# Kernel optimization log

Hardware: AMD Instinct MI355X
Metric: run time of the kernel (lower is better)

The kernel has to match this reference:

```python
import jax, jax.numpy as jnp
import numpy as np

EPS = 1e-5  # torch GroupNorm default eps


def gn(x, g, b):
    # GroupNorm with 1 group on [N, C]: normalize over channel dim per row
    mu = jnp.mean(x, axis=-1, keepdims=True)
    var = jnp.var(x, axis=-1, keepdims=True)
    return (x - mu) * jax.lax.rsqrt(var + EPS) * g + b


def setup_inputs() -> dict:
    N, A, E, D = 500000, 20000, 500000, 128
    key = jax.random.key(0)
    ks = jax.random.split(key, 12)
    s = 0.05
    return {
        "map_x": jax.random.normal(ks[0], (N, 8), jnp.float32),
        "agt_x": jax.random.normal(ks[1], (A, 80), jnp.float32),
        "u": jax.random.randint(ks[2], (E,), 0, A),
        "v": jax.random.randint(ks[3], (E,), 0, N),
        # map_fc: Linear(8,D) with bias, then custom Linear(D,D,bias=False)+GN+ReLU
        "W0": jax.random.normal(ks[4], (D, 8), jnp.float32) * s,
        "b0": jnp.zeros((D,), jnp.float32),
        "W1": jax.random.normal(ks[5], (D, D), jnp.float32) * s,
        "g1": jnp.ones((D,), jnp.float32),
        "b1": jnp.zeros((D,), jnp.float32),
        # agt_fc: Linear(80, D, bias=False)
        "Wa": jax.random.normal(ks[6], (D, 80), jnp.float32) * s,
        # self.bn GroupNorm params
        "g_bn": jnp.ones((D,), jnp.float32),
        "b_bn": jnp.zeros((D,), jnp.float32),
        # self.fc: Linear(2D, D, bias=False)+GN+ReLU
        "Wf": jax.random.normal(ks[7], (D, 2 * D), jnp.float32) * s,
        "g_fc": jnp.ones((D,), jnp.float32),
        "b_fc": jnp.zeros((D,), jnp.float32),
    }


def reference(map_x, agt_x, u, v, W0, b0, W1, g1, b1, Wa, g_bn, b_bn, Wf, g_fc, b_fc):
    # map_fc: Linear+ReLU, then Linear(no bias)+GN+ReLU
    h = jax.nn.relu(map_x @ W0.T + b0)                      # [N, D]
    h = jax.nn.relu(gn(h @ W1.T, g1, b1))                   # [N, D]
    # agent messages: project agents once (A < E), then gather per edge
    msg = (agt_x @ Wa.T)[u]                                 # [E, D]
    tmp = jnp.zeros_like(h).at[v].add(msg)                  # scatter-add into map nodes
    tmp = jax.nn.relu(gn(tmp, g_bn, b_bn))                  # [N, D]
    cat = jnp.concatenate([h, tmp], axis=-1)                # [N, 2D]
    out = jax.nn.relu(gn(cat @ Wf.T, g_fc, b_fc))           # [N, D]
    return out
```

## Files before the change

kernel.cpp:

```cpp
#include <hip/hip_runtime.h>
#include <stdint.h>

#define EPS 1e-5f

typedef short bh8 __attribute__((ext_vector_type(8)));
typedef float f4v __attribute__((ext_vector_type(4)));
typedef unsigned short ushort_t;

static __device__ __forceinline__ unsigned short f2bf(float f) {
    unsigned u = __builtin_bit_cast(unsigned, f);
    u += 0x7fffu + ((u >> 16) & 1u);
    return (unsigned short)(u >> 16);
}

static __device__ __forceinline__ float bfbits(unsigned x) {
    return __builtin_bit_cast(float, x);
}

static __device__ __forceinline__ void acc16(float* tv, uint4 qa, uint4 qb) {
    unsigned wd[8] = {qa.x, qa.y, qa.z, qa.w, qb.x, qb.y, qb.z, qb.w};
#pragma unroll
    for (int p = 0; p < 8; ++p) {
        tv[2 * p + 0] += bfbits(wd[p] << 16);
        tv[2 * p + 1] += bfbits(wd[p] & 0xffff0000u);
    }
}


__global__ void prep(const float* __restrict__ W1, const float* __restrict__ Wf,
                     const float* __restrict__ Wa, ushort_t* __restrict__ W1b,
                     ushort_t* __restrict__ Wfb, float* __restrict__ WaT) {
    int i = blockIdx.x * 256 + threadIdx.x;
    if (i < 16384) W1b[i] = f2bf(W1[i]);
    else if (i < 49152) { int j = i - 16384; Wfb[j] = f2bf(Wf[j]); }
    else if (i < 59392) { int l2 = i - 49152; int k = l2 >> 7, c = l2 & 127; WaT[l2] = Wa[c * 80 + k]; }
}

__global__ __launch_bounds__(256) void proj_agents(const float* __restrict__ agt,
                                                   const float* __restrict__ WaT,
                                                   unsigned short* __restrict__ Pb) {
    __shared__ float WT[80 * 128];
    __shared__ float xT[80][32];
    int t = threadIdx.x;
    int row0 = blockIdx.x * 32;
#pragma unroll
    for (int m = 0; m < 40; ++m) WT[t + 256 * m] = WaT[t + 256 * m];
#pragma unroll
    for (int m = 0; m < 10; ++m) {
        int f = t + 256 * m;
        int r = f / 80, k = f - r * 80;
        xT[k][r] = agt[(size_t)(row0 + r) * 80 + k];
    }
    __syncthreads();
    int tx = t & 31, ty = t >> 5;
    float acc[4][4] = {};
    for (int k = 0; k < 80; ++k) {
        float4 xv = *(const float4*)&xT[k][ty * 4];
        float4 wv = *(const float4*)&WT[k * 128 + tx * 4];
        float xa[4] = {xv.x, xv.y, xv.z, xv.w};
        float wa[4] = {wv.x, wv.y, wv.z, wv.w};
#pragma unroll
        for (int i = 0; i < 4; ++i)
#pragma unroll
            for (int j = 0; j < 4; ++j) acc[i][j] = fmaf(xa[i], wa[j], acc[i][j]);
    }
#pragma unroll
    for (int i = 0; i < 4; ++i) {
        int r = row0 + ty * 4 + i;
        union { unsigned short s[4]; uint2 q; } o;
#pragma unroll
        for (int j = 0; j < 4; ++j) o.s[j] = f2bf(acc[i][j]);
        *(uint2*)&Pb[(size_t)r * 128 + tx * 4] = o.q;
    }
}

__global__ void hist_v(const int* __restrict__ v, int* __restrict__ cnt, int E) {
    int e = blockIdx.x * 256 + threadIdx.x;
    if (e < E) atomicAdd(&cnt[v[e]], 1);
}

__global__ __launch_bounds__(256) void scan1(const int* __restrict__ cnt,
                                             int* __restrict__ rp,
                                             int* __restrict__ partials, int n) {
    __shared__ int lds[256];
    int b = blockIdx.x, t = threadIdx.x;
    int base = b * 4096 + t * 16;
    int vv[16];
    int run = 0;
#pragma unroll
    for (int i = 0; i < 16; ++i) {
        int c = (base + i < n) ? cnt[base + i] : 0;
        vv[i] = run;
        run += c;
    }
    lds[t] = run;
    __syncthreads();
#pragma unroll
    for (int off = 1; off < 256; off <<= 1) {
        int x = (t >= off) ? lds[t - off] : 0;
        __syncthreads();
        lds[t] += x;
        __syncthreads();
    }
    int excl = lds[t] - run;
    if (t == 255) partials[b] = lds[255];
#pragma unroll
    for (int i = 0; i < 16; ++i)
        if (base + i < n) rp[base + i] = excl + vv[i];
}

__global__ __launch_bounds__(256) void scan2(int* __restrict__ partials, int nb) {
    __shared__ int lds[256];
    int t = threadIdx.x;
    int vv = (t < nb) ? partials[t] : 0;
    lds[t] = vv;
    __syncthreads();
#pragma unroll
    for (int off = 1; off < 256; off <<= 1) {
        int x = (t >= off) ? lds[t - off] : 0;
        __syncthreads();
        lds[t] += x;
        __syncthreads();
    }
    if (t < nb) partials[t] = lds[t] - vv;
}

__global__ void scan3(int* __restrict__ rp, const int* __restrict__ partials,
                      int n, int E) {
    int i = blockIdx.x * 256 + threadIdx.x;
    if (i < n) rp[i] += partials[i >> 12];
    if (i == 0) rp[n] = E;
}

__global__ void fill_csr(const int* __restrict__ u, const int* __restrict__ v,
                         const int* __restrict__ rp, int* __restrict__ cursor,
                         int* __restrict__ col, int E) {
    int e = blockIdx.x * 256 + threadIdx.x;
    if (e < E) {
        int vv = v[e];
        int pos = rp[vv] + atomicAdd(&cursor[vv], 1);
        col[pos] = u[e];
    }
}

__global__ __launch_bounds__(256) void gather_gn(
    const unsigned short* __restrict__ Pb, const int* __restrict__ rp,
    const int* __restrict__ col, const float* __restrict__ g_bn,
    const float* __restrict__ b_bn, ushort_t* __restrict__ catB) {
    const int t = threadIdx.x;
    const int node = blockIdx.x * 32 + (t >> 3);
    const int c0 = (t & 7) * 16;
    const int beg = rp[node];
    const int deg = rp[node + 1] - beg;
    const int ca = col[(deg > 0) ? beg : 0];
    const int cb = col[(deg > 1) ? beg + 1 : 0];
    const int cc = col[(deg > 2) ? beg + 2 : 0];
    const int cd = col[(deg > 3) ? beg + 3 : 0];
    const unsigned short* pB = Pb + c0;
    float tv[16] = {};
    if (deg > 0) { const uint4* p = (const uint4*)(pB + (size_t)ca * 128); acc16(tv, p[0], p[1]); }
    if (deg > 1) { const uint4* p = (const uint4*)(pB + (size_t)cb * 128); acc16(tv, p[0], p[1]); }
    if (deg > 2) { const uint4* p = (const uint4*)(pB + (size_t)cc * 128); acc16(tv, p[0], p[1]); }
    if (deg > 3) { const uint4* p = (const uint4*)(pB + (size_t)cd * 128); acc16(tv, p[0], p[1]); }
    for (int k = 4; k < deg; ++k) {
        const uint4* p = (const uint4*)(pB + (size_t)col[beg + k] * 128);
        acc16(tv, p[0], p[1]);
    }
    float a = 0.f, q = 0.f;
#pragma unroll
    for (int i = 0; i < 16; ++i) { a += tv[i]; q += tv[i] * tv[i]; }
#pragma unroll
    for (int msk = 1; msk < 8; msk <<= 1) {
        a += __shfl_xor(a, msk, 64);
        q += __shfl_xor(q, msk, 64);
    }
    const float mean = a * (1.f / 128.f);
    const float var = q * (1.f / 128.f) - mean * mean;
    const float inv = rsqrtf(var + EPS);
    union { unsigned short s[16]; uint4 q4[2]; } o;
#pragma unroll
    for (int i = 0; i < 16; ++i) {
        const int cch = c0 + i;
        o.s[i] = f2bf(fmaxf((tv[i] - mean) * inv * g_bn[cch] + b_bn[cch], 0.f));
    }
    uint4* dst = (uint4*)(catB + (size_t)node * 128 + c0);
    dst[0] = o.q4[0];
    dst[1] = o.q4[1];
}

__global__ __launch_bounds__(512, 4) void fused(
    const float* __restrict__ mapx, const float* __restrict__ W0,
    const float* __restrict__ b0, const ushort_t* __restrict__ W1b,
    const float* __restrict__ g1, const float* __restrict__ b1,
    const ushort_t* __restrict__ catB, const ushort_t* __restrict__ Wfb,
    const float* __restrict__ g_fc, const float* __restrict__ b_fc,
    float* __restrict__ out, int ntiles)
{
    __shared__ __align__(16) short h0sA[32 * 128], h0sB[32 * 128];
    __shared__ __align__(16) short catsA[32 * 256], catsB[32 * 256];
    __shared__ float W0s[128 * 8];
    __shared__ float b0s[128];
    __shared__ float2 partA[8][32], partB[8][32];
    __shared__ float gA[128], bA[128], gC[128], bC[128];

    const int t = threadIdx.x;
    const int w = t >> 6;
    const int l = t & 63;
    const int l15 = l & 15, lg = l >> 4;

    if (t < 128) {
        gA[t] = g1[t];   bA[t] = b1[t];
        gC[t] = g_fc[t]; bC[t] = b_fc[t];
        b0s[t] = b0[t];
    }
    for (int i = t; i < 1024; i += 512) W0s[i] = W0[i];

    bh8 w1b[4], wfb[8];
    {
        const int wr = 16 * w + l15;
#pragma unroll
        for (int s = 0; s < 4; ++s)
            w1b[s] = *(const bh8*)(W1b + (size_t)wr * 128 + s * 32 + lg * 8);
#pragma unroll
        for (int s = 0; s < 8; ++s)
            wfb[s] = *(const bh8*)(Wfb + (size_t)wr * 256 + s * 32 + lg * 8);
    }
    __syncthreads();

    const f4v fzero = {0.f, 0.f, 0.f, 0.f};
    const int stride = (int)gridDim.x;
    const int npairs = (ntiles + 1) >> 1;

    for (int j = blockIdx.x; j < npairs; j += stride) {
        const int tileA = 2 * j, tileB = 2 * j + 1;
        const bool hasB = (tileB < ntiles);
        const int rowA0 = tileA * 32, rowB0 = tileB * 32;

        {
            const int r = t & 31, cg = t >> 5;
            const int ad = (r * 256 + cg * 16) ^ ((r & 7) << 4);
            {
                float mx[8];
                const float* p = mapx + (size_t)(rowA0 + r) * 8;
                *(float4*)&mx[0] = *(const float4*)p;
                *(float4*)&mx[4] = *(const float4*)(p + 4);
                __align__(16) unsigned short hb[8];
#pragma unroll
                for (int c = 0; c < 8; ++c) {
                    const int cc = 8 * cg + c;
                    float a = b0s[cc];
#pragma unroll
                    for (int jj = 0; jj < 8; ++jj) a = fmaf(mx[jj], W0s[cc * 8 + jj], a);
                    hb[c] = f2bf(fmaxf(a, 0.f));
                }
                *(uint4*)((char*)h0sA + ad) = *(const uint4*)&hb[0];
            }
            if (hasB) {
                float mx[8];
                const float* p = mapx + (size_t)(rowB0 + r) * 8;
                *(float4*)&mx[0] = *(const float4*)p;
                *(float4*)&mx[4] = *(const float4*)(p + 4);
                __align__(16) unsigned short hb[8];
#pragma unroll
                for (int c = 0; c < 8; ++c) {
                    const int cc = 8 * cg + c;
                    float a = b0s[cc];
#pragma unroll
                    for (int jj = 0; jj < 8; ++jj) a = fmaf(mx[jj], W0s[cc * 8 + jj], a);
                    hb[c] = f2bf(fmaxf(a, 0.f));
                }
                *(uint4*)((char*)h0sB + ad) = *(const uint4*)&hb[0];
            }
        }
        {
            const int r2 = t >> 4, cb = (t & 15) * 8;
            const int ad = (r2 * 512 + 256 + cb * 2) ^ ((r2 & 7) << 4);
            uint4 qa = *(const uint4*)(catB + (size_t)(rowA0 + r2) * 128 + cb);
            *(uint4*)((char*)catsA + ad) = qa;
            if (hasB) {
                uint4 qb = *(const uint4*)(catB + (size_t)(rowB0 + r2) * 128 + cb);
                *(uint4*)((char*)catsB + ad) = qb;
            }
        }
        __syncthreads();

        f4v a2A[2], a2B[2];
        a2A[0] = fzero; a2A[1] = fzero; a2B[0] = fzero; a2B[1] = fzero;
#pragma unroll
        for (int s = 0; s < 4; ++s) {
            bh8 afA[2], afB[2];
#pragma unroll
            for (int m = 0; m < 2; ++m) {
                const int row = 16 * m + l15;
                const int a = (row * 256 + s * 64 + lg * 16) ^ ((row & 7) << 4);
                afA[m] = *(const bh8*)((const char*)h0sA + a);
                afB[m] = *(const bh8*)((const char*)h0sB + a);
            }
#pragma unroll
            for (int m = 0; m < 2; ++m) {
                a2A[m] = __builtin_amdgcn_mfma_f32_16x16x32_bf16(w1b[s], afA[m], a2A[m], 0, 0, 0);
                a2B[m] = __builtin_amdgcn_mfma_f32_16x16x32_bf16(w1b[s], afB[m], a2B[m], 0, 0, 0);
            }
        }

#pragma unroll
        for (int m = 0; m < 2; ++m) {
            float aA = a2A[m][0] + a2A[m][1] + a2A[m][2] + a2A[m][3];
            float qA = a2A[m][0] * a2A[m][0] + a2A[m][1] * a2A[m][1] +
                       a2A[m][2] * a2A[m][2] + a2A[m][3] * a2A[m][3];
            float aB = a2B[m][0] + a2B[m][1] + a2B[m][2] + a2B[m][3];
            float qB = a2B[m][0] * a2B[m][0] + a2B[m][1] * a2B[m][1] +
                       a2B[m][2] * a2B[m][2] + a2B[m][3] * a2B[m][3];
            aA += __shfl_xor(aA, 16, 64); qA += __shfl_xor(qA, 16, 64);
            aA += __shfl_xor(aA, 32, 64); qA += __shfl_xor(qA, 32, 64);
            aB += __shfl_xor(aB, 16, 64); qB += __shfl_xor(qB, 16, 64);
            aB += __shfl_xor(aB, 32, 64); qB += __shfl_xor(qB, 32, 64);
            if (lg == 0) {
                partA[w][16 * m + l15] = make_float2(aA, qA);
                partB[w][16 * m + l15] = make_float2(aB, qB);
            }
        }
        __syncthreads();

#pragma unroll
        for (int m = 0; m < 2; ++m) {
            const int row = 16 * m + l15;
            const int c00 = 16 * w + 4 * lg;
            const int ad = (row * 512 + c00 * 2) ^ ((row & 7) << 4);
            {
                float a = 0.f, q = 0.f;
#pragma unroll
                for (int pw = 0; pw < 8; ++pw) {
                    float2 pq = partA[pw][row];
                    a += pq.x; q += pq.y;
                }
                const float mean = a * (1.f / 128.f);
                const float var = q * (1.f / 128.f) - mean * mean;
                const float inv = rsqrtf(var + EPS);
                union { unsigned short s[4]; uint2 q2; } o;
#pragma unroll
                for (int reg = 0; reg < 4; ++reg) {
                    float v2 = (a2A[m][reg] - mean) * inv * gA[c00 + reg] + bA[c00 + reg];
                    o.s[reg] = f2bf(fmaxf(v2, 0.f));
                }
                *(uint2*)((char*)catsA + ad) = o.q2;
            }
            {
                float a = 0.f, q = 0.f;
#pragma unroll
                for (int pw = 0; pw < 8; ++pw) {
                    float2 pq = partB[pw][row];
                    a += pq.x; q += pq.y;
                }
                const float mean = a * (1.f / 128.f);
                const float var = q * (1.f / 128.f) - mean * mean;
                const float inv = rsqrtf(var + EPS);
                union { unsigned short s[4]; uint2 q2; } o;
#pragma unroll
                for (int reg = 0; reg < 4; ++reg) {
                    float v2 = (a2B[m][reg] - mean) * inv * gA[c00 + reg] + bA[c00 + reg];
                    o.s[reg] = f2bf(fmaxf(v2, 0.f));
                }
                *(uint2*)((char*)catsB + ad) = o.q2;
            }
        }
        __syncthreads();

        f4v a3A[2], a3B[2];
        a3A[0] = fzero; a3A[1] = fzero; a3B[0] = fzero; a3B[1] = fzero;
#pragma unroll
        for (int s = 0; s < 8; ++s) {
            bh8 afA[2], afB[2];
#pragma unroll
            for (int m = 0; m < 2; ++m) {
                const int row = 16 * m + l15;
                const int a = (row * 512 + s * 64 + lg * 16) ^ ((row & 7) << 4);
                afA[m] = *(const bh8*)((const char*)catsA + a);
                afB[m] = *(const bh8*)((const char*)catsB + a);
            }
#pragma unroll
            for (int m = 0; m < 2; ++m) {
                a3A[m] = __builtin_amdgcn_mfma_f32_16x16x32_bf16(wfb[s], afA[m], a3A[m], 0, 0, 0);
                a3B[m] = __builtin_amdgcn_mfma_f32_16x16x32_bf16(wfb[s], afB[m], a3B[m], 0, 0, 0);
            }
        }

#pragma unroll
        for (int m = 0; m < 2; ++m) {
            float aA = a3A[m][0] + a3A[m][1] + a3A[m][2] + a3A[m][3];
            float qA = a3A[m][0] * a3A[m][0] + a3A[m][1] * a3A[m][1] +
                       a3A[m][2] * a3A[m][2] + a3A[m][3] * a3A[m][3];
            float aB = a3B[m][0] + a3B[m][1] + a3B[m][2] + a3B[m][3];
            float qB = a3B[m][0] * a3B[m][0] + a3B[m][1] * a3B[m][1] +
                       a3B[m][2] * a3B[m][2] + a3B[m][3] * a3B[m][3];
            aA += __shfl_xor(aA, 16, 64); qA += __shfl_xor(qA, 16, 64);
            aA += __shfl_xor(aA, 32, 64); qA += __shfl_xor(qA, 32, 64);
            aB += __shfl_xor(aB, 16, 64); qB += __shfl_xor(qB, 16, 64);
            aB += __shfl_xor(aB, 32, 64); qB += __shfl_xor(qB, 32, 64);
            if (lg == 0) {
                partA[w][16 * m + l15] = make_float2(aA, qA);
                partB[w][16 * m + l15] = make_float2(aB, qB);
            }
        }
        __syncthreads();

#pragma unroll
        for (int m = 0; m < 2; ++m) {
            const int row = 16 * m + l15;
            const int c00 = 16 * w + 4 * lg;
            {
                float a = 0.f, q = 0.f;
#pragma unroll
                for (int pw = 0; pw < 8; ++pw) {
                    float2 pq = partA[pw][row];
                    a += pq.x; q += pq.y;
                }
                const float mean = a * (1.f / 128.f);
                const float var = q * (1.f / 128.f) - mean * mean;
                const float inv = rsqrtf(var + EPS);
                float4 o;
                o.x = fmaxf((a3A[m][0] - mean) * inv * gC[c00 + 0] + bC[c00 + 0], 0.f);
                o.y = fmaxf((a3A[m][1] - mean) * inv * gC[c00 + 1] + bC[c00 + 1], 0.f);
                o.z = fmaxf((a3A[m][2] - mean) * inv * gC[c00 + 2] + bC[c00 + 2], 0.f);
                o.w = fmaxf((a3A[m][3] - mean) * inv * gC[c00 + 3] + bC[c00 + 3], 0.f);
                *(float4*)&out[(size_t)(rowA0 + row) * 128 + c00] = o;
            }
            if (hasB) {
                float a = 0.f, q = 0.f;
#pragma unroll
                for (int pw = 0; pw < 8; ++pw) {
                    float2 pq = partB[pw][row];
                    a += pq.x; q += pq.y;
                }
                const float mean = a * (1.f / 128.f);
                const float var = q * (1.f / 128.f) - mean * mean;
                const float inv = rsqrtf(var + EPS);
                float4 o;
                o.x = fmaxf((a3B[m][0] - mean) * inv * gC[c00 + 0] + bC[c00 + 0], 0.f);
                o.y = fmaxf((a3B[m][1] - mean) * inv * gC[c00 + 1] + bC[c00 + 1], 0.f);
                o.z = fmaxf((a3B[m][2] - mean) * inv * gC[c00 + 2] + bC[c00 + 2], 0.f);
                o.w = fmaxf((a3B[m][3] - mean) * inv * gC[c00 + 3] + bC[c00 + 3], 0.f);
                *(float4*)&out[(size_t)(rowB0 + row) * 128 + c00] = o;
            }
        }
    }
}

extern "C" void kernel_launch(void* const* d_in, const int* in_sizes, int n_in,
                              void* d_out, int out_size, void* d_ws, size_t ws_size,
                              hipStream_t stream) {
    const float* mapx = (const float*)d_in[0];
    const float* agt  = (const float*)d_in[1];
    const int*   u    = (const int*)d_in[2];
    const int*   v    = (const int*)d_in[3];
    const float* W0   = (const float*)d_in[4];
    const float* b0   = (const float*)d_in[5];
    const float* W1   = (const float*)d_in[6];
    const float* g1   = (const float*)d_in[7];
    const float* b1   = (const float*)d_in[8];
    const float* Wa   = (const float*)d_in[9];
    const float* g_bn = (const float*)d_in[10];
    const float* b_bn = (const float*)d_in[11];
    const float* Wf   = (const float*)d_in[12];
    const float* g_fc = (const float*)d_in[13];
    const float* b_fc = (const float*)d_in[14];
    int N = in_sizes[0] / 8;
    int A = in_sizes[1] / 80;
    int E = in_sizes[2];
    float* out = (float*)d_out;

    char* ws = (char*)d_ws;
    unsigned short* Pb  = (unsigned short*)(ws + 0);
    float*    WaT       = (float*)(ws + 5120000);
    ushort_t* W1b       = (ushort_t*)(ws + 5160960);
    ushort_t* Wfb       = (ushort_t*)(ws + 5193728);
    int*      cnt       = (int*)(ws + 5259264);
    int*      cursor    = (int*)(ws + 7259264);
    int*      rp        = (int*)(ws + 9259264);
    int*      partials  = (int*)(ws + 11259392);
    int*      colv      = (int*)(ws + 11261440);
    ushort_t* catB      = (ushort_t*)(ws + 16777216);

    const int nb_scan = (N + 4095) / 4096;
    const int nb_e = (E + 255) / 256;

    prep<<<232, 256, 0, stream>>>(W1, Wf, Wa, W1b, Wfb, WaT);
    hipMemsetAsync(cnt, 0, 4000000, stream);
    hist_v<<<nb_e, 256, 0, stream>>>(v, cnt, E);
    proj_agents<<<A / 32, 256, 0, stream>>>(agt, WaT, Pb);
    scan1<<<nb_scan, 256, 0, stream>>>(cnt, rp, partials, N);
    scan2<<<1, 256, 0, stream>>>(partials, nb_scan);
    scan3<<<(N + 255) / 256, 256, 0, stream>>>(rp, partials, N, E);
    fill_csr<<<nb_e, 256, 0, stream>>>(u, v, rp, cursor, colv, E);
    gather_gn<<<N / 32, 256, 0, stream>>>(Pb, rp, colv, g_bn, b_bn, catB);

    int ntiles = N / 32;
    fused<<<512, 512, 0, stream>>>(mapx, W0, b0, W1b, g1, b1, catB,
                                   Wfb, g_fc, b_fc, out, ntiles);
}
```

Baseline: 349.1 us.

## Load scatter operand fragments directly from global and reduce GN stats with LDS atomics

The tmp (scatter-aggregated) half of the concatenated input is no longer staged through shared memory. Each wave now loads its MFMA operand fragments straight from global catB, and the cats buffers shrink to hold only the h half. The per-wave partial sum arrays for the GroupNorm statistics are replaced by shared-memory float atomics into per-row sum and sum-of-squares slots, so the 8-way partial reduction loops go away. This cuts LDS footprint and one staging pass, but each 128-channel row is now read redundantly by all 8 waves from global/L2, and the atomics add contention and ordering nondeterminism.

```diff
diff --git a/kernel.cpp b/kernel.cpp
--- a/kernel.cpp
+++ b/kernel.cpp
@@ -197,10 +197,10 @@
     float* __restrict__ out, int ntiles)
 {
     __shared__ __align__(16) short h0sA[32 * 128], h0sB[32 * 128];
-    __shared__ __align__(16) short catsA[32 * 256], catsB[32 * 256];
+    __shared__ __align__(16) short catsA[32 * 128], catsB[32 * 128];
     __shared__ float W0s[128 * 8];
     __shared__ float b0s[128];
-    __shared__ float2 partA[8][32], partB[8][32];
+    __shared__ float S2[2][32], Q2[2][32], S3[2][32], Q3[2][32];
     __shared__ float gA[128], bA[128], gC[128], bC[128];
 
     const int t = threadIdx.x;
@@ -236,6 +236,7 @@
         const bool hasB = (tileB < ntiles);
         const int rowA0 = tileA * 32, rowB0 = tileB * 32;
 
+        if (t < 64) { ((float*)S2)[t] = 0.f; ((float*)Q2)[t] = 0.f; }
         {
             const int r = t & 31, cg = t >> 5;
             const int ad = (r * 256 + cg * 16) ^ ((r & 7) << 4);
@@ -272,18 +273,9 @@
                 *(uint4*)((char*)h0sB + ad) = *(const uint4*)&hb[0];
             }
         }
-        {
-            const int r2 = t >> 4, cb = (t & 15) * 8;
-            const int ad = (r2 * 512 + 256 + cb * 2) ^ ((r2 & 7) << 4);
-            uint4 qa = *(const uint4*)(catB + (size_t)(rowA0 + r2) * 128 + cb);
-            *(uint4*)((char*)catsA + ad) = qa;
-            if (hasB) {
-                uint4 qb = *(const uint4*)(catB + (size_t)(rowB0 + r2) * 128 + cb);
-                *(uint4*)((char*)catsB + ad) = qb;
-            }
-        }
-        __syncthreads();
-
+        __syncthreads();
+
+        if (t < 64) { ((float*)S3)[t] = 0.f; ((float*)Q3)[t] = 0.f; }
         f4v a2A[2], a2B[2];
         a2A[0] = fzero; a2A[1] = fzero; a2B[0] = fzero; a2B[1] = fzero;
 #pragma unroll
@@ -302,7 +294,6 @@
                 a2B[m] = __builtin_amdgcn_mfma_f32_16x16x32_bf16(w1b[s], afB[m], a2B[m], 0, 0, 0);
             }
         }
-
 #pragma unroll
         for (int m = 0; m < 2; ++m) {
             float aA = a2A[m][0] + a2A[m][1] + a2A[m][2] + a2A[m][3];
@@ -316,8 +307,11 @@
             aB += __shfl_xor(aB, 16, 64); qB += __shfl_xor(qB, 16, 64);
             aB += __shfl_xor(aB, 32, 64); qB += __shfl_xor(qB, 32, 64);
             if (lg == 0) {
-                partA[w][16 * m + l15] = make_float2(aA, qA);
-                partB[w][16 * m + l15] = make_float2(aB, qB);
+                const int row = 16 * m + l15;
+                atomicAdd(&S2[0][row], aA);
+                atomicAdd(&Q2[0][row], qA);
+                atomicAdd(&S2[1][row], aB);
+                atomicAdd(&Q2[1][row], qB);
             }
         }
         __syncthreads();
@@ -326,14 +320,9 @@
         for (int m = 0; m < 2; ++m) {
             const int row = 16 * m + l15;
             const int c00 = 16 * w + 4 * lg;
-            const int ad = (row * 512 + c00 * 2) ^ ((row & 7) << 4);
+            const int ad = (row * 256 + c00 * 2) ^ ((row & 7) << 4);
             {
-                float a = 0.f, q = 0.f;
-#pragma unroll
-                for (int pw = 0; pw < 8; ++pw) {
-                    float2 pq = partA[pw][row];
-                    a += pq.x; q += pq.y;
-                }
+                const float a = S2[0][row], q = Q2[0][row];
                 const float mean = a * (1.f / 128.f);
                 const float var = q * (1.f / 128.f) - mean * mean;
                 const float inv = rsqrtf(var + EPS);
@@ -346,12 +335,7 @@
                 *(uint2*)((char*)catsA + ad) = o.q2;
             }
             {
-                float a = 0.f, q = 0.f;
-#pragma unroll
-                for (int pw = 0; pw < 8; ++pw) {
-                    float2 pq = partB[pw][row];
-                    a += pq.x; q += pq.y;
-                }
+                const float a = S2[1][row], q = Q2[1][row];
                 const float mean = a * (1.f / 128.f);
                 const float var = q * (1.f / 128.f) - mean * mean;
                 const float inv = rsqrtf(var + EPS);
@@ -369,22 +353,41 @@
         f4v a3A[2], a3B[2];
         a3A[0] = fzero; a3A[1] = fzero; a3B[0] = fzero; a3B[1] = fzero;
 #pragma unroll
-        for (int s = 0; s < 8; ++s) {
-            bh8 afA[2], afB[2];
+        for (int m = 0; m < 2; ++m) {
+            const int row = 16 * m + l15;
+            bh8 mf[4];
+            const ushort_t* pbase = catB + (size_t)(rowA0 + row) * 128 + lg * 8;
+#pragma unroll
+            for (int s = 0; s < 4; ++s) mf[s] = *(const bh8*)(pbase + s * 32);
+#pragma unroll
+            for (int s = 0; s < 4; ++s) {
+                const int a = (row * 256 + s * 64 + lg * 16) ^ ((row & 7) << 4);
+                bh8 af = *(const bh8*)((const char*)catsA + a);
+                a3A[m] = __builtin_amdgcn_mfma_f32_16x16x32_bf16(wfb[s], af, a3A[m], 0, 0, 0);
+            }
+#pragma unroll
+            for (int s = 0; s < 4; ++s)
+                a3A[m] = __builtin_amdgcn_mfma_f32_16x16x32_bf16(wfb[4 + s], mf[s], a3A[m], 0, 0, 0);
+        }
+        if (hasB) {
 #pragma unroll
             for (int m = 0; m < 2; ++m) {
                 const int row = 16 * m + l15;
-                const int a = (row * 512 + s * 64 + lg * 16) ^ ((row & 7) << 4);
-                afA[m] = *(const bh8*)((const char*)catsA + a);
-                afB[m] = *(const bh8*)((const char*)catsB + a);
-            }
-#pragma unroll
-            for (int m = 0; m < 2; ++m) {
-                a3A[m] = __builtin_amdgcn_mfma_f32_16x16x32_bf16(wfb[s], afA[m], a3A[m], 0, 0, 0);
-                a3B[m] = __builtin_amdgcn_mfma_f32_16x16x32_bf16(wfb[s], afB[m], a3B[m], 0, 0, 0);
-            }
-        }
-
+                bh8 mf[4];
+                const ushort_t* pbase = catB + (size_t)(rowB0 + row) * 128 + lg * 8;
+#pragma unroll
+                for (int s = 0; s < 4; ++s) mf[s] = *(const bh8*)(pbase + s * 32);
+#pragma unroll
+                for (int s = 0; s < 4; ++s) {
+                    const int a = (row * 256 + s * 64 + lg * 16) ^ ((row & 7) << 4);
+                    bh8 af = *(const bh8*)((const char*)catsB + a);
+                    a3B[m] = __builtin_amdgcn_mfma_f32_16x16x32_bf16(wfb[s], af, a3B[m], 0, 0, 0);
+                }
+#pragma unroll
+                for (int s = 0; s < 4; ++s)
+                    a3B[m] = __builtin_amdgcn_mfma_f32_16x16x32_bf16(wfb[4 + s], mf[s], a3B[m], 0, 0, 0);
+            }
+        }
 #pragma unroll
         for (int m = 0; m < 2; ++m) {
             float aA = a3A[m][0] + a3A[m][1] + a3A[m][2] + a3A[m][3];
@@ -398,8 +401,11 @@
             aB += __shfl_xor(aB, 16, 64); qB += __shfl_xor(qB, 16, 64);
             aB += __shfl_xor(aB, 32, 64); qB += __shfl_xor(qB, 32, 64);
             if (lg == 0) {
-                partA[w][16 * m + l15] = make_float2(aA, qA);
-                partB[w][16 * m + l15] = make_float2(aB, qB);
+                const int row = 16 * m + l15;
+                atomicAdd(&S3[0][row], aA);
+                atomicAdd(&Q3[0][row], qA);
+                atomicAdd(&S3[1][row], aB);
+                atomicAdd(&Q3[1][row], qB);
             }
         }
         __syncthreads();
@@ -409,12 +415,7 @@
             const int row = 16 * m + l15;
             const int c00 = 16 * w + 4 * lg;
             {
-                float a = 0.f, q = 0.f;
-#pragma unroll
-                for (int pw = 0; pw < 8; ++pw) {
-                    float2 pq = partA[pw][row];
-                    a += pq.x; q += pq.y;
-                }
+                const float a = S3[0][row], q = Q3[0][row];
                 const float mean = a * (1.f / 128.f);
                 const float var = q * (1.f / 128.f) - mean * mean;
                 const float inv = rsqrtf(var + EPS);
@@ -426,12 +427,7 @@
                 *(float4*)&out[(size_t)(rowA0 + row) * 128 + c00] = o;
             }
             if (hasB) {
-                float a = 0.f, q = 0.f;
-#pragma unroll
-                for (int pw = 0; pw < 8; ++pw) {
-                    float2 pq = partB[pw][row];
-                    a += pq.x; q += pq.y;
-                }
+                const float a = S3[1][row], q = Q3[1][row];
                 const float mean = a * (1.f / 128.f);
                 const float var = q * (1.f / 128.f) - mean * mean;
                 const float inv = rsqrtf(var + EPS);
```

Result: slower. 404.9 us (+16.0%).
